# Optimization experiments

Hardware: AMD Instinct MI355X
Metric: run time of the kernel (lower is better)

## Reference

```python
import jax, jax.numpy as jnp
import numpy as np

KH = KW = 3
STRIDE = 1
PAD = 1
DIL = 1


def im2col(x, kh, kw, stride, pad, dil):
    """F.unfold equivalent: x (N,C,H,W) -> (N,C,kh,kw,oh,ow)."""
    n, c, h, w = x.shape
    oh = (h + 2 * pad - dil * (kh - 1) - 1) // stride + 1
    ow = (w + 2 * pad - dil * (kw - 1) - 1) // stride + 1
    xp = jnp.pad(x, ((0, 0), (0, 0), (pad, pad), (pad, pad)))
    rows = []
    for i in range(kh):
        cols = []
        for j in range(kw):
            patch = jax.lax.slice(
                xp,
                (0, 0, i * dil, j * dil),
                (n, c, i * dil + (oh - 1) * stride + 1, j * dil + (ow - 1) * stride + 1),
                (1, 1, stride, stride),
            )  # (N,C,oh,ow)
            cols.append(patch)
        rows.append(jnp.stack(cols, axis=2))  # (N,C,kw,oh,ow)
    return jnp.stack(rows, axis=2)  # (N,C,kh,kw,oh,ow)


def setup_inputs() -> dict:
    key = jax.random.key(0)
    k1, k2, k3, k4 = jax.random.split(key, 4)
    N, Cin, Cout, H, W = 4, 64, 64, 128, 128
    x = jax.random.normal(k1, (N, Cin, H, W), dtype=jnp.float32)
    # adapting kernel: positive values (softmax-like output in EdgeKernel2d)
    kernel = jax.random.uniform(k2, (N, 1, KH, KW, H, W), dtype=jnp.float32, minval=0.01, maxval=1.0)
    fan_in = Cin * KH * KW
    weight = jax.random.normal(k3, (Cout, Cin, KH, KW), dtype=jnp.float32) * (1.0 / np.sqrt(fan_in))
    bias = jax.random.normal(k4, (Cout,), dtype=jnp.float32) * 0.01
    return {"x": x, "kernel": kernel, "weight": weight, "bias": bias}


def reference(x, kernel, weight, bias):
    # im_cols: (N,Cin,kh,kw,oh,ow)
    im_cols = im2col(x, KH, KW, STRIDE, PAD, DIL)
    in_mul_k = im_cols * kernel  # kernel broadcasts over Cin
    # dominate = sum_{k,l} in_mul_k / sum_{k,l} kernel  -> (N,Cin,oh,ow)
    dominate = in_mul_k.sum(axis=(2, 3)) / kernel.sum(axis=(2, 3))
    corrected = in_mul_k + dominate[:, :, None, None] * (1.0 - kernel)
    out = jnp.einsum('ncklhw,ockl->nohw', corrected, weight)
    out = out + bias[None, :, None, None]
    return out
```

## Files before the change

### kernel.cpp

```cpp
#include <hip/hip_runtime.h>
#include <hip/hip_bf16.h>
#include <cstddef>

typedef __attribute__((ext_vector_type(8))) short bf16x8;
typedef __attribute__((ext_vector_type(4))) float f32x4;
typedef __attribute__((ext_vector_type(2))) unsigned int u32x2;

#define NB 4
#define CIN 64
#define COUT 64
#define HH 128
#define WW 128
#define TAPS 9
#define STRD 82

__device__ __forceinline__ unsigned short f2bf(float f) {
    union { float f; unsigned u; } v; v.f = f;
    unsigned u = v.u + 0x7FFFu + ((v.u >> 16) & 1u);
    return (unsigned short)(u >> 16);
}

__global__ void prep_weight(const float* __restrict__ w, unsigned short* __restrict__ wBv) {
    int idx = blockIdx.x * blockDim.x + threadIdx.x;
    if (idx >= 40960) return;
    int e    = idx & 7;
    int lane = (idx >> 3) & 63;
    int fid  = idx >> 9;
    int wv   = fid / 20;
    int rem  = fid - wv * 20;
    int chunk = rem / 5;
    int step  = rem - chunk * 5;
    int l15 = lane & 15, g = lane >> 4;
    int o  = wv * 16 + l15;
    int kk = step * 32 + g * 8 + e;
    unsigned short v = 0;
    if (kk < 144) {
        int tap = kk >> 4;
        int cl  = kk & 15;
        v = f2bf(w[(o * CIN + chunk * 16 + cl) * TAPS + tap]);
    }
    wBv[idx] = v;
}

__launch_bounds__(256)
__global__ void pac_conv(const float* __restrict__ x, const float* __restrict__ Kp,
                         const unsigned short* __restrict__ wBv,
                         const float* __restrict__ bias,
                         float* __restrict__ out) {
    __shared__ unsigned int sCor[64][STRD];

    const int blk0 = blockIdx.x;
    const int blk  = ((blk0 & 7) << 7) | (blk0 >> 3);

    const int w0 = (blk & 1) * 64;
    const int h  = (blk >> 1) & (HH - 1);
    const int n  = blk >> 8;
    const int t    = threadIdx.x;
    const int lane = t & 63;
    const int wv   = __builtin_amdgcn_readfirstlane(t >> 6);

    const bool mL = (w0 == 0) && (lane == 0);
    const bool mR = (w0 != 0) && (lane == 63);
    const unsigned voffL = (mL ? 1u : (unsigned)lane) * 4u;
    const unsigned voffC = ((unsigned)lane + 1u) * 4u;
    const unsigned voffR = (mR ? 64u : (unsigned)lane + 2u) * 4u;

    auto load_x = [&](int chunk, float (&xv)[4][TAPS]) {
        const int c0 = chunk * 16 + wv * 4;
        const float* xb = x + (size_t)(n * CIN + c0) * (HH * WW) + w0 - 1;
        #pragma unroll
        for (int j = 0; j < 4; ++j) {
            #pragma unroll
            for (int k = 0; k < 3; ++k) {
                const int hh2 = h + k - 1;
                const bool hok = (unsigned)hh2 < (unsigned)HH;
                const int hc = hok ? hh2 : (hh2 < 0 ? 0 : HH - 1);
                const float* p = xb + (size_t)j * (HH * WW) + (size_t)hc * WW;
                float vL = *(const float*)((const char*)p + voffL);
                float vC = *(const float*)((const char*)p + voffC);
                float vR = *(const float*)((const char*)p + voffR);
                xv[j][k * 3 + 0] = (hok && !mL) ? vL : 0.f;
                xv[j][k * 3 + 1] = hok ? vC : 0.f;
                xv[j][k * 3 + 2] = (hok && !mR) ? vR : 0.f;
            }
        }
    };

    float xv0[4][TAPS];
    load_x(0, xv0);

    float kreg[TAPS];
    float ks = 0.f;
    const float* kp = Kp + ((size_t)n * TAPS * HH + h) * WW + w0 + lane;
    #pragma unroll
    for (int tap = 0; tap < TAPS; ++tap) {
        kreg[tap] = kp[(size_t)tap * HH * WW];
        ks += kreg[tap];
    }
    const float inv = 1.0f / ks;

    for (int i = t; i < 64 * 8; i += 256) sCor[i >> 3][72 + (i & 7)] = 0u;

    const int l15 = lane & 15;
    const int g   = lane >> 4;
    const float bval = bias[wv * 16 + l15];

    f32x4 acc[4];
    #pragma unroll
    for (int i = 0; i < 4; ++i) acc[i] = (f32x4){0.f, 0.f, 0.f, 0.f};

    #pragma unroll
    for (int chunk = 0; chunk < 4; ++chunk) {
        float xv[4][TAPS];
        if (chunk == 0) {
            #pragma unroll
            for (int j = 0; j < 4; ++j)
                #pragma unroll
                for (int tap = 0; tap < TAPS; ++tap) xv[j][tap] = xv0[j][tap];
        } else {
            load_x(chunk, xv);
        }

        float dom[4];
        #pragma unroll
        for (int j = 0; j < 4; ++j) {
            float s = 0.f;
            #pragma unroll
            for (int tap = 0; tap < TAPS; ++tap) s = fmaf(xv[j][tap], kreg[tap], s);
            dom[j] = s * inv;
        }
        u32x2 cor[TAPS];
        #pragma unroll
        for (int tap = 0; tap < TAPS; ++tap) {
            float c0f = fmaf(kreg[tap], xv[0][tap] - dom[0], dom[0]);
            float c1f = fmaf(kreg[tap], xv[1][tap] - dom[1], dom[1]);
            float c2f = fmaf(kreg[tap], xv[2][tap] - dom[2], dom[2]);
            float c3f = fmaf(kreg[tap], xv[3][tap] - dom[3], dom[3]);
            union { __hip_bfloat162 h2; unsigned int u; } a, b;
            a.h2 = __float22bfloat162_rn(make_float2(c0f, c1f));
            b.h2 = __float22bfloat162_rn(make_float2(c2f, c3f));
            cor[tap] = (u32x2){a.u, b.u};
        }

        if (chunk) __syncthreads();
        #pragma unroll
        for (int tap = 0; tap < TAPS; ++tap)
            *reinterpret_cast<u32x2*>(&sCor[lane][tap * 8 + wv * 2]) = cor[tap];
        __syncthreads();

        const unsigned short* wfb =
            wBv + (((size_t)(wv * 20 + chunk * 5) << 6) + lane) * 8;
        #pragma unroll
        for (int step = 0; step < 5; ++step) {
            bf16x8 bfrag = *reinterpret_cast<const bf16x8*>(wfb + (step << 9));
            #pragma unroll
            for (int pt = 0; pt < 4; ++pt) {
                const unsigned int* ap = &sCor[pt * 16 + l15][step * 16 + g * 4];
                u32x2 alo = *reinterpret_cast<const u32x2*>(ap);
                u32x2 ahi = *reinterpret_cast<const u32x2*>(ap + 2);
                union { u32x2 p[2]; bf16x8 f; } af;
                af.p[0] = alo; af.p[1] = ahi;
                acc[pt] = __builtin_amdgcn_mfma_f32_16x16x32_bf16(af.f, bfrag, acc[pt], 0, 0, 0);
            }
        }
    }

    const int o = wv * 16 + l15;
    float* op = out + (((size_t)n * COUT + o) * HH + h) * WW + w0 + g * 4;
    #pragma unroll
    for (int pt = 0; pt < 4; ++pt) {
        f32x4 v = acc[pt];
        #pragma unroll
        for (int r = 0; r < 4; ++r) v[r] += bval;
        *reinterpret_cast<f32x4*>(op + pt * 16) = v;
    }
}

extern "C" void kernel_launch(void* const* d_in, const int* in_sizes, int n_in,
                              void* d_out, int out_size, void* d_ws, size_t ws_size,
                              hipStream_t stream) {
    const float* x    = (const float*)d_in[0];
    const float* Kp   = (const float*)d_in[1];
    const float* wgt  = (const float*)d_in[2];
    const float* bias = (const float*)d_in[3];
    float* out = (float*)d_out;
    unsigned short* wBv = (unsigned short*)d_ws;

    prep_weight<<<160, 256, 0, stream>>>(wgt, wBv);

    pac_conv<<<NB * HH * (WW / 64), 256, 0, stream>>>(x, Kp, wBv, bias, out);
}
```

Before: 28.86 us.

## Shrink pixel tile to 32 and split channels across half-waves

Each block now handles 32 output pixels instead of 64, which doubles the grid. Each half-wave handles a pair of input channels instead of each wave handling four, so per-thread register state (x taps, corrections, accumulators) roughly halves. Launch bounds request 8 blocks per SM to raise occupancy and hide global-load latency. In exchange, the weight fragments and the K values of neighbouring pixels are reloaded across twice as many blocks, and each MFMA B fragment is reused for fewer A tiles.

```diff
diff --git a/kernel.cpp b/kernel.cpp
--- a/kernel.cpp
+++ b/kernel.cpp
@@ -42,34 +42,62 @@
     wBv[idx] = v;
 }
 
-__launch_bounds__(256)
+__launch_bounds__(256, 8)
 __global__ void pac_conv(const float* __restrict__ x, const float* __restrict__ Kp,
                          const unsigned short* __restrict__ wBv,
                          const float* __restrict__ bias,
                          float* __restrict__ out) {
-    __shared__ unsigned int sCor[64][STRD];
+    __shared__ unsigned int sCor[32][STRD];
 
     const int blk0 = blockIdx.x;
-    const int blk  = ((blk0 & 7) << 7) | (blk0 >> 3);
+    const int blk  = ((blk0 & 7) << 8) | (blk0 >> 3);
 
-    const int w0 = (blk & 1) * 64;
-    const int h  = (blk >> 1) & (HH - 1);
-    const int n  = blk >> 8;
+    const int w0 = (blk & 3) * 32;
+    const int h  = (blk >> 2) & (HH - 1);
+    const int n  = blk >> 9;
+
     const int t    = threadIdx.x;
     const int lane = t & 63;
     const int wv   = __builtin_amdgcn_readfirstlane(t >> 6);
+    const int px   = lane & 31;
+    const int cpair = t >> 5;
 
-    const bool mL = (w0 == 0) && (lane == 0);
-    const bool mR = (w0 != 0) && (lane == 63);
-    const unsigned voffL = (mL ? 1u : (unsigned)lane) * 4u;
-    const unsigned voffC = ((unsigned)lane + 1u) * 4u;
-    const unsigned voffR = (mR ? 64u : (unsigned)lane + 2u) * 4u;
+    float kreg[TAPS];
+    float ks = 0.f;
+    const float* kp = Kp + ((size_t)n * TAPS * HH + h) * WW + w0 + px;
+    #pragma unroll
+    for (int tap = 0; tap < TAPS; ++tap) {
+        kreg[tap] = kp[(size_t)tap * HH * WW];
+        ks += kreg[tap];
+    }
+    const float inv = 1.0f / ks;
 
-    auto load_x = [&](int chunk, float (&xv)[4][TAPS]) {
-        const int c0 = chunk * 16 + wv * 4;
+    sCor[t >> 3][72 + (t & 7)] = 0u;
+
+    const bool mL = (w0 == 0)  && (px == 0);
+    const bool mR = (w0 == 96) && (px == 31);
+    const unsigned voffL = (mL ? 1u : (unsigned)px) * 4u;
+    const unsigned voffC = ((unsigned)px + 1u) * 4u;
+    const unsigned voffR = (mR ? (unsigned)px : (unsigned)px + 2u) * 4u;
+
+    const int l15 = lane & 15;
+    const int g   = lane >> 4;
+    const float bval = bias[wv * 16 + l15];
+
+    f32x4 acc[2];
+    acc[0] = (f32x4){0.f, 0.f, 0.f, 0.f};
+    acc[1] = (f32x4){0.f, 0.f, 0.f, 0.f};
+
+    #pragma unroll
+    for (int chunk = 0; chunk < 4; ++chunk) {
+        const int c0 = chunk * 16 + cpair * 2;
         const float* xb = x + (size_t)(n * CIN + c0) * (HH * WW) + w0 - 1;
+
+        unsigned int cor[TAPS];
+        float cprev[TAPS];
         #pragma unroll
-        for (int j = 0; j < 4; ++j) {
+        for (int j = 0; j < 2; ++j) {
+            float xv[TAPS];
             #pragma unroll
             for (int k = 0; k < 3; ++k) {
                 const int hh2 = h + k - 1;
@@ -79,73 +107,33 @@
                 float vL = *(const float*)((const char*)p + voffL);
                 float vC = *(const float*)((const char*)p + voffC);
                 float vR = *(const float*)((const char*)p + voffR);
-                xv[j][k * 3 + 0] = (hok && !mL) ? vL : 0.f;
-                xv[j][k * 3 + 1] = hok ? vC : 0.f;
-                xv[j][k * 3 + 2] = (hok && !mR) ? vR : 0.f;
+                xv[k * 3 + 0] = (hok && !mL) ? vL : 0.f;
+                xv[k * 3 + 1] = hok ? vC : 0.f;
+                xv[k * 3 + 2] = (hok && !mR) ? vR : 0.f;
             }
-        }
-    };
-
-    float xv0[4][TAPS];
-    load_x(0, xv0);
-
-    float kreg[TAPS];
-    float ks = 0.f;
-    const float* kp = Kp + ((size_t)n * TAPS * HH + h) * WW + w0 + lane;
-    #pragma unroll
-    for (int tap = 0; tap < TAPS; ++tap) {
-        kreg[tap] = kp[(size_t)tap * HH * WW];
-        ks += kreg[tap];
-    }
-    const float inv = 1.0f / ks;
-
-    for (int i = t; i < 64 * 8; i += 256) sCor[i >> 3][72 + (i & 7)] = 0u;
-
-    const int l15 = lane & 15;
-    const int g   = lane >> 4;
-    const float bval = bias[wv * 16 + l15];
-
-    f32x4 acc[4];
-    #pragma unroll
-    for (int i = 0; i < 4; ++i) acc[i] = (f32x4){0.f, 0.f, 0.f, 0.f};
-
-    #pragma unroll
-    for (int chunk = 0; chunk < 4; ++chunk) {
-        float xv[4][TAPS];
-        if (chunk == 0) {
-            #pragma unroll
-            for (int j = 0; j < 4; ++j)
-                #pragma unroll
-                for (int tap = 0; tap < TAPS; ++tap) xv[j][tap] = xv0[j][tap];
-        } else {
-            load_x(chunk, xv);
-        }
-
-        float dom[4];
-        #pragma unroll
-        for (int j = 0; j < 4; ++j) {
             float s = 0.f;
             #pragma unroll
-            for (int tap = 0; tap < TAPS; ++tap) s = fmaf(xv[j][tap], kreg[tap], s);
-            dom[j] = s * inv;
-        }
-        u32x2 cor[TAPS];
-        #pragma unroll
-        for (int tap = 0; tap < TAPS; ++tap) {
-            float c0f = fmaf(kreg[tap], xv[0][tap] - dom[0], dom[0]);
-            float c1f = fmaf(kreg[tap], xv[1][tap] - dom[1], dom[1]);
-            float c2f = fmaf(kreg[tap], xv[2][tap] - dom[2], dom[2]);
-            float c3f = fmaf(kreg[tap], xv[3][tap] - dom[3], dom[3]);
-            union { __hip_bfloat162 h2; unsigned int u; } a, b;
-            a.h2 = __float22bfloat162_rn(make_float2(c0f, c1f));
-            b.h2 = __float22bfloat162_rn(make_float2(c2f, c3f));
-            cor[tap] = (u32x2){a.u, b.u};
+            for (int tap = 0; tap < TAPS; ++tap) s = fmaf(xv[tap], kreg[tap], s);
+            const float d = s * inv;
+            if (j == 0) {
+                #pragma unroll
+                for (int tap = 0; tap < TAPS; ++tap)
+                    cprev[tap] = fmaf(kreg[tap], xv[tap] - d, d);
+            } else {
+                #pragma unroll
+                for (int tap = 0; tap < TAPS; ++tap) {
+                    float cc = fmaf(kreg[tap], xv[tap] - d, d);
+                    union { __hip_bfloat162 h2; unsigned int u; } pk;
+                    pk.h2 = __float22bfloat162_rn(make_float2(cprev[tap], cc));
+                    cor[tap] = pk.u;
+                }
+            }
         }
 
         if (chunk) __syncthreads();
         #pragma unroll
         for (int tap = 0; tap < TAPS; ++tap)
-            *reinterpret_cast<u32x2*>(&sCor[lane][tap * 8 + wv * 2]) = cor[tap];
+            sCor[px][tap * 8 + cpair] = cor[tap];
         __syncthreads();
 
         const unsigned short* wfb =
@@ -154,7 +142,7 @@
         for (int step = 0; step < 5; ++step) {
             bf16x8 bfrag = *reinterpret_cast<const bf16x8*>(wfb + (step << 9));
             #pragma unroll
-            for (int pt = 0; pt < 4; ++pt) {
+            for (int pt = 0; pt < 2; ++pt) {
                 const unsigned int* ap = &sCor[pt * 16 + l15][step * 16 + g * 4];
                 u32x2 alo = *reinterpret_cast<const u32x2*>(ap);
                 u32x2 ahi = *reinterpret_cast<const u32x2*>(ap + 2);
@@ -168,7 +156,7 @@
     const int o = wv * 16 + l15;
     float* op = out + (((size_t)n * COUT + o) * HH + h) * WW + w0 + g * 4;
     #pragma unroll
-    for (int pt = 0; pt < 4; ++pt) {
+    for (int pt = 0; pt < 2; ++pt) {
         f32x4 v = acc[pt];
         #pragma unroll
         for (int r = 0; r < 4; ++r) v[r] += bval;
@@ -188,5 +176,5 @@
 
     prep_weight<<<160, 256, 0, stream>>>(wgt, wBv);
 
-    pac_conv<<<NB * HH * (WW / 64), 256, 0, stream>>>(x, Kp, wBv, bias, out);
+    pac_conv<<<NB * HH * (WW / 32), 256, 0, stream>>>(x, Kp, wBv, bias, out);
 }
```

New measurement: 28.91 us. About the same (+0.2%).
